# Optimization experiments

Measured on AMD Instinct MI355X. Metric: run time of the kernel, lower is better.

Reference implementation:

```python
import jax, jax.numpy as jnp
import numpy as np

B, L, IN, OUT = 32, 2048, 192, 2
H, N2, NL = 512, 32, 4  # hidden_dim, d_state//2 complex modes, num_layers


def setup_inputs() -> dict:
    key = jax.random.key(0)
    ks = jax.random.split(key, 8)
    neural_input = jax.random.normal(ks[0], (B, L, IN), jnp.float32)
    W_in = jax.random.normal(ks[1], (IN, H), jnp.float32) / np.sqrt(IN)
    b_in = jnp.zeros((H,), jnp.float32)
    # S4D kernel params (stacked over layers)
    log_dt = jax.random.uniform(ks[2], (NL, H), jnp.float32, np.log(1e-3), np.log(1e-1))
    Cri = jax.random.normal(ks[3], (NL, H, N2, 2), jnp.float32)  # complex C as (re, im)
    log_A_real = jnp.full((NL, H, N2), np.log(0.5), jnp.float32)
    A_imag = jnp.broadcast_to(np.pi * jnp.arange(N2, dtype=np.float32), (NL, H, N2)).astype(jnp.float32)
    D = jax.random.normal(ks[4], (NL, H), jnp.float32)
    # position-wise output conv1x1 producing 2H channels for GLU
    conv_w = jax.random.normal(ks[5], (NL, 2 * H, H), jnp.float32) / np.sqrt(H)
    conv_b = jnp.zeros((NL, 2 * H), jnp.float32)
    W_out = jax.random.normal(ks[6], (H, OUT), jnp.float32) / np.sqrt(H)
    b_out = jnp.zeros((OUT,), jnp.float32)
    return dict(neural_input=neural_input, W_in=W_in, b_in=b_in, log_dt=log_dt,
                Cri=Cri, log_A_real=log_A_real, A_imag=A_imag, D=D,
                conv_w=conv_w, conv_b=conv_b, W_out=W_out, b_out=b_out)


def _s4d_layer(u, log_dt, Cri, log_A_real, A_imag, D, conv_w, conv_b):
    # u: (B, H, L)
    Lx = u.shape[-1]
    dt = jnp.exp(log_dt)[:, None]                       # (H, 1)
    C = Cri[..., 0] + 1j * Cri[..., 1]                  # (H, N2) complex
    A = -jnp.exp(log_A_real) + 1j * A_imag              # (H, N2)
    dtA = A * dt                                        # (H, N2)
    Ct = C * (jnp.exp(dtA) - 1.0) / A                   # (H, N2)
    # Vandermonde kernel: K[h, l] = 2 Re sum_n Ct[h,n] exp(dtA[h,n] * l)
    vand = jnp.exp(dtA[..., None] * jnp.arange(Lx))     # (H, N2, L) complex
    K = 2.0 * jnp.einsum('hn,hnl->hl', Ct, vand).real   # (H, L)
    # circular conv via FFT at length 2L (== linear conv, causal)
    k_f = jnp.fft.rfft(K, n=2 * Lx)
    u_f = jnp.fft.rfft(u, n=2 * Lx)
    y = jnp.fft.irfft(u_f * k_f, n=2 * Lx)[..., :Lx]    # (B, H, L)
    y = y + u * D[:, None]
    y = jax.nn.gelu(y, approximate=False)               # torch nn.GELU (erf)
    # conv1x1 to 2H channels + GLU over channel dim
    z = jnp.einsum('oh,bhl->bol', conv_w, y) + conv_b[None, :, None]
    a, b = jnp.split(z, 2, axis=1)
    return a * jax.nn.sigmoid(b)


def reference(neural_input, W_in, b_in, log_dt, Cri, log_A_real, A_imag, D,
              conv_w, conv_b, W_out, b_out):
    x = neural_input @ W_in + b_in          # (B, L, H)
    u = jnp.transpose(x, (0, 2, 1))         # (B, H, L) channels-first for SSM
    for i in range(NL):
        u = _s4d_layer(u, log_dt[i], Cri[i], log_A_real[i], A_imag[i],
                       D[i], conv_w[i], conv_b[i])
    y = jnp.transpose(u, (0, 2, 1))         # (B, L, H)
    return y @ W_out + b_out                # (B, L, OUT)
```

## Files before the change

### kernel.cpp

```cpp
#include <hip/hip_runtime.h>
#include <hip/hip_bf16.h>
#include <math.h>

#define BB 32
#define LL 2048
#define INP 192
#define OUTC 2
#define HH 512
#define NN2 32
#define NNL 4
#define TABB 32768

using short8 = __attribute__((ext_vector_type(8))) short;
using f32x4  = __attribute__((ext_vector_type(4))) float;
using f32x2  = __attribute__((ext_vector_type(2))) float;

__device__ __forceinline__ float sigmoidf_(float x) {
  return 1.0f / (1.0f + expf(-x));
}
__device__ __forceinline__ unsigned short bf16bits(float x) {
  __hip_bfloat16 b = __float2bfloat16(x);
  return __builtin_bit_cast(unsigned short, b);
}
__device__ __forceinline__ float bfval(unsigned short b) {
  unsigned int u = (unsigned int)b << 16;
  return __builtin_bit_cast(float, u);
}
__device__ __forceinline__ float gelu_fast(float x) {
  float s = x * 0.70710678118654752f;
  float ax = fabsf(s);
  float tt = 1.0f / fmaf(0.3275911f, ax, 1.0f);
  float p = fmaf(1.061405429f, tt, -1.453152027f);
  p = fmaf(p, tt, 1.421413741f);
  p = fmaf(p, tt, -0.284496736f);
  p = fmaf(p, tt, 0.254829592f);
  float e = __expf(-s * s);
  float er = 1.0f - p * tt * e;
  er = copysignf(er, s);
  return 0.5f * x * (1.0f + er);
}
__device__ __forceinline__ void gload16(const void* gsrc, void* ldst) {
  __builtin_amdgcn_global_load_lds(
      (const __attribute__((address_space(1))) void*)gsrc,
      (__attribute__((address_space(3))) void*)ldst, 16, 0, 0);
}

__global__ __launch_bounds__(256) void k_params(const float* __restrict__ log_dt,
                                                const float* __restrict__ Cri,
                                                const float* __restrict__ lAr,
                                                const float* __restrict__ Aim,
                                                float* __restrict__ P) {
  int idx = blockIdx.x * 256 + threadIdx.x;
  if (idx >= NNL * HH * NN2) return;
  float dt  = expf(log_dt[idx / NN2]);
  float Are = -expf(lAr[idx]);
  float Aimv = Aim[idx];
  float dre = Are * dt, dim = Aimv * dt;
  float er = expf(dre);
  float wrv = er * cosf(dim);
  float wiv = er * sinf(dim);
  float Er = wrv - 1.0f, Ei = wiv;
  float den = Are * Are + Aimv * Aimv;
  float Fr = (Er * Are + Ei * Aimv) / den;
  float Fi = (Ei * Are - Er * Aimv) / den;
  float Cre = Cri[idx * 2 + 0], Cim = Cri[idx * 2 + 1];
  P[idx * 4 + 0] = wrv;
  P[idx * 4 + 1] = wiv;
  P[idx * 4 + 2] = 2.0f * (Cre * Fr - Cim * Fi);
  P[idx * 4 + 3] = 2.0f * (Cre * Fi + Cim * Fr);
}

__global__ __launch_bounds__(64) void k_tables(const float* __restrict__ P,
                                               char* __restrict__ Tab) {
  __shared__ float kk[32];
  int tid = threadIdx.x;
  int lh = blockIdx.x;
  char* tb = Tab + (size_t)lh * TABB;
  if (tid < 32) {
    int n = tid;
    const float4 pq = reinterpret_cast<const float4*>(P)[(size_t)lh * NN2 + n];
    float wr = pq.x, wi = pq.y, c2r = pq.z, c2i = pq.w;
    int mt = n >> 4;
    float pr = 1.0f, pi = 0.0f;
    for (int d = 0; d < 32; ++d) {
      {
        int t_ = 31 - d;
        int lane = ((t_ >> 3) << 4) + (n & 15);
        int j = t_ & 7;
        unsigned short hr = bf16bits(pr);
        unsigned short lr = bf16bits(pr - bfval(hr));
        unsigned short hi_ = bf16bits(pi);
        unsigned short li_ = bf16bits(pi - bfval(hi_));
        *(unsigned short*)(tb + (mt * 2 + 0) * 1024 + lane * 16 + j * 2) = hr;
        *(unsigned short*)(tb + (mt * 2 + 1) * 1024 + lane * 16 + j * 2) = hi_;
        *(unsigned short*)(tb + 4096 + (mt * 2 + 0) * 1024 + lane * 16 + j * 2) = lr;
        *(unsigned short*)(tb + 4096 + (mt * 2 + 1) * 1024 + lane * 16 + j * 2) = li_;
      }
      {
        int mtT = d >> 4;
        int lane = (((n & 15) >> 2) << 4) + (d & 15);
        int jre = n & 3, jim = (n & 3) + 4;
        unsigned short hr = bf16bits(pr);
        unsigned short lr = bf16bits(pr - bfval(hr));
        float nim = -pi;
        unsigned short hi_ = bf16bits(nim);
        unsigned short li_ = bf16bits(nim - bfval(hi_));
        char* bh = tb + 8192 + (mtT * 2 + mt) * 1024 + lane * 16;
        char* bl = tb + 12288 + (mtT * 2 + mt) * 1024 + lane * 16;
        *(unsigned short*)(bh + jre * 2) = hr;
        *(unsigned short*)(bh + jim * 2) = hi_;
        *(unsigned short*)(bl + jre * 2) = lr;
        *(unsigned short*)(bl + jim * 2) = li_;
      }
      float kp = c2r * pr - c2i * pi;
      #pragma unroll
      for (int k = 1; k < 32; k <<= 1) kp += __shfl_xor(kp, k, 32);
      if (n == 0) kk[d] = kp;
      float nr = pr * wr - pi * wi;
      pi = pr * wi + pi * wr;
      pr = nr;
    }
    float w32r = pr, w32i = pi;
    float c2wr = c2r * wr - c2i * wi;
    float c2wi = c2r * wi + c2i * wr;
    int s = ((n >> 4) << 2) + (n & 3);
    int gg = (n & 15) >> 2;
    float pmr = 1.0f, pmi = 0.0f;
    for (int m = 0; m < 16; ++m) {
      float* q = (float*)(tb + 20480 + (size_t)((s * 64) + (gg * 16 + m)) * 24);
      q[0] = w32r; q[1] = w32i; q[2] = pmr; q[3] = pmi; q[4] = c2wr; q[5] = c2wi;
      float t2 = pmr * w32r - pmi * w32i;
      pmi = pmr * w32i + pmi * w32r;
      pmr = t2;
    }
  }
  __syncthreads();
  for (int idx = tid; idx < 1024; idx += 64) {
    int mt = idx >> 9, rem = idx & 511;
    int lane = rem >> 3, j = rem & 7;
    int tt = (mt << 4) + (lane & 15);
    int jf = ((lane >> 4) << 3) + j;
    float val = (jf <= tt) ? kk[tt - jf] : 0.0f;
    unsigned short hb = bf16bits(val);
    unsigned short lb = bf16bits(val - bfval(hb));
    *(unsigned short*)(tb + 16384 + mt * 1024 + lane * 16 + j * 2) = hb;
    *(unsigned short*)(tb + 18432 + mt * 1024 + lane * 16 + j * 2) = lb;
  }
}

__global__ __launch_bounds__(256) void k_tobf16(const float* __restrict__ src,
                                                __hip_bfloat16* __restrict__ dst,
                                                int n) {
  int i = (blockIdx.x * 256 + threadIdx.x) * 4;
  if (i >= n) return;
  float4 v = *reinterpret_cast<const float4*>(&src[i]);
  dst[i + 0] = __float2bfloat16(v.x);
  dst[i + 1] = __float2bfloat16(v.y);
  dst[i + 2] = __float2bfloat16(v.z);
  dst[i + 3] = __float2bfloat16(v.w);
}

__global__ __launch_bounds__(256) void k_splitx(const float* __restrict__ src,
                                                __hip_bfloat16* __restrict__ hi,
                                                __hip_bfloat16* __restrict__ lo,
                                                int n) {
  int i = (blockIdx.x * 256 + threadIdx.x) * 4;
  if (i >= n) return;
  float4 v = *reinterpret_cast<const float4*>(&src[i]);
  float vv[4] = {v.x, v.y, v.z, v.w};
  unsigned short hb[4], lb[4];
  #pragma unroll
  for (int j = 0; j < 4; ++j) {
    hb[j] = bf16bits(vv[j]);
    lb[j] = bf16bits(vv[j] - bfval(hb[j]));
  }
  *reinterpret_cast<uint2*>(hi + i) = make_uint2(
      (unsigned)hb[0] | ((unsigned)hb[1] << 16), (unsigned)hb[2] | ((unsigned)hb[3] << 16));
  *reinterpret_cast<uint2*>(lo + i) = make_uint2(
      (unsigned)lb[0] | ((unsigned)lb[1] << 16), (unsigned)lb[2] | ((unsigned)lb[3] << 16));
}

__global__ __launch_bounds__(256) void k_prepwt(const float* __restrict__ W,
                                                __hip_bfloat16* __restrict__ hi,
                                                __hip_bfloat16* __restrict__ lo) {
  int idx = blockIdx.x * 256 + threadIdx.x;
  if (idx >= HH * INP) return;
  int h = idx / INP, k = idx - h * INP;
  float v = W[(size_t)k * HH + h];
  unsigned short hb = bf16bits(v);
  hi[idx] = __builtin_bit_cast(__hip_bfloat16, hb);
  lo[idx] = __float2bfloat16(v - bfval(hb));
}

__global__ __launch_bounds__(256) void k_ingemm(const __hip_bfloat16* __restrict__ Xhi,
                                                const __hip_bfloat16* __restrict__ Xlo,
                                                const __hip_bfloat16* __restrict__ Wthi,
                                                const __hip_bfloat16* __restrict__ Wtlo,
                                                const float* __restrict__ bias,
                                                float* __restrict__ U) {
  int lt = blockIdx.x * 128;
  int ht = blockIdx.y * 128;
  int b  = blockIdx.z;
  int t = threadIdx.x;
  int wid = t >> 6, lane = t & 63;
  int wrow = wid >> 1, wcol = wid & 1;
  int l15 = lane & 15, g = lane >> 4;

  const short* Xh = (const short*)Xhi + (size_t)b * LL * INP;
  const short* Xl = (const short*)Xlo + (size_t)b * LL * INP;
  const short* Bh = (const short*)Wthi;
  const short* Bl = (const short*)Wtlo;

  f32x4 acc[4][4];
  #pragma unroll
  for (int m = 0; m < 4; ++m)
    #pragma unroll
    for (int n = 0; n < 4; ++n) acc[m][n] = f32x4{0.f, 0.f, 0.f, 0.f};

  int lbase = lt + wrow * 64 + l15;
  int hbase = ht + wcol * 64 + l15;

  #pragma unroll
  for (int ks = 0; ks < 6; ++ks) {
    int k0 = ks * 32 + 8 * g;
    short8 ah[4], al[4], bh[4], bl[4];
    #pragma unroll
    for (int m = 0; m < 4; ++m) {
      size_t off = (size_t)(lbase + m * 16) * INP + k0;
      ah[m] = *reinterpret_cast<const short8*>(Xh + off);
      al[m] = *reinterpret_cast<const short8*>(Xl + off);
    }
    #pragma unroll
    for (int n = 0; n < 4; ++n) {
      size_t off = (size_t)(hbase + n * 16) * INP + k0;
      bh[n] = *reinterpret_cast<const short8*>(Bh + off);
      bl[n] = *reinterpret_cast<const short8*>(Bl + off);
    }
    #pragma unroll
    for (int m = 0; m < 4; ++m)
      #pragma unroll
      for (int n = 0; n < 4; ++n) {
        acc[m][n] = __builtin_amdgcn_mfma_f32_16x16x32_bf16(ah[m], bh[n], acc[m][n], 0, 0, 0);
        acc[m][n] = __builtin_amdgcn_mfma_f32_16x16x32_bf16(ah[m], bl[n], acc[m][n], 0, 0, 0);
        acc[m][n] = __builtin_amdgcn_mfma_f32_16x16x32_bf16(al[m], bh[n], acc[m][n], 0, 0, 0);
      }
  }

  #pragma unroll
  for (int n = 0; n < 4; ++n) {
    int h = hbase + n * 16;
    float bv = bias[h];
    #pragma unroll
    for (int m = 0; m < 4; ++m) {
      int l0 = lt + wrow * 64 + m * 16 + g * 4;
      float4 o;
      o.x = acc[m][n][0] + bv;
      o.y = acc[m][n][1] + bv;
      o.z = acc[m][n][2] + bv;
      o.w = acc[m][n][3] + bv;
      *reinterpret_cast<float4*>(&U[((size_t)b * HH + h) * LL + l0]) = o;
    }
  }
}

__global__ __launch_bounds__(512) void k_scan(const float* __restrict__ U,
                                              short* __restrict__ Ybt,
                                              const char* __restrict__ Tab,
                                              const float* __restrict__ Dp) {
  __shared__ short ylds[8 * 2048];
  int t = threadIdx.x;
  int lane = t & 63;
  int wid = t >> 6;
  int row = __builtin_amdgcn_readfirstlane(blockIdx.x * 8 + wid);
  int h = row & (HH - 1);
  const char* tb = Tab + (size_t)h * TABB;
  const float* urow = U + (size_t)row * LL;
  int g = lane >> 4, m = lane & 15;

  short8 uh[4], ul[4];
  #pragma unroll
  for (int c0 = 0; c0 < 4; ++c0) {
    const float* p = urow + 512 * c0 + 32 * m + 8 * g;
    float4 va = *reinterpret_cast<const float4*>(p);
    float4 vb = *reinterpret_cast<const float4*>(p + 4);
    float v[8] = {va.x, va.y, va.z, va.w, vb.x, vb.y, vb.z, vb.w};
    short8 hi, lo;
    #pragma unroll
    for (int j = 0; j < 8; ++j) {
      unsigned short hb = bf16bits(v[j]);
      hi[j] = (short)hb;
      lo[j] = (short)bf16bits(v[j] - bfval(hb));
    }
    uh[c0] = hi;
    ul[c0] = lo;
  }

  f32x4 Z[2][2][4];
  #pragma unroll
  for (int mt = 0; mt < 2; ++mt)
    #pragma unroll
    for (int reim = 0; reim < 2; ++reim) {
      short8 whi = *reinterpret_cast<const short8*>(tb + (mt * 2 + reim) * 1024 + lane * 16);
      short8 wlo = *reinterpret_cast<const short8*>(tb + 4096 + (mt * 2 + reim) * 1024 + lane * 16);
      #pragma unroll
      for (int c0 = 0; c0 < 4; ++c0) {
        f32x4 z = {0.f, 0.f, 0.f, 0.f};
        z = __builtin_amdgcn_mfma_f32_16x16x32_bf16(whi, uh[c0], z, 0, 0, 0);
        z = __builtin_amdgcn_mfma_f32_16x16x32_bf16(whi, ul[c0], z, 0, 0, 0);
        z = __builtin_amdgcn_mfma_f32_16x16x32_bf16(wlo, uh[c0], z, 0, 0, 0);
        Z[mt][reim][c0] = z;
      }
    }

  float aR[8][4], aI[8][4];
  #pragma unroll
  for (int s = 0; s < 8; ++s) {
    int mt = s >> 2, i = s & 3;
    const char* plb = tb + 20480 + (size_t)(s * 64 + lane) * 24;
    f32x2 w32 = *reinterpret_cast<const f32x2*>(plb);
    f32x2 w32m = *reinterpret_cast<const f32x2*>(plb + 8);
    f32x2 c2w = *reinterpret_cast<const f32x2*>(plb + 16);
    float r1r = w32[0], r1i = w32[1];
    float r2r = r1r * r1r - r1i * r1i, r2i = 2.f * r1r * r1i;
    float r4r = r2r * r2r - r2i * r2i, r4i = 2.f * r2r * r2i;
    float r8r = r4r * r4r - r4i * r4i, r8i = 2.f * r4r * r4i;
    float w16r = r8r * r8r - r8i * r8i, w16i = 2.f * r8r * r8i;

    float Er[4], Ei[4], Tr[4], Ti[4];
    #pragma unroll
    for (int c0 = 0; c0 < 4; ++c0) {
      float Pr = Z[mt][0][c0][i], Pi = Z[mt][1][c0][i];
      {
        float qr = __shfl_up(Pr, 1u, 16), qi = __shfl_up(Pi, 1u, 16);
        if (m < 1) { qr = 0.f; qi = 0.f; }
        Pr = fmaf(r1r, qr, fmaf(-r1i, qi, Pr));
        Pi = fmaf(r1r, qi, fmaf(r1i, qr, Pi));
      }
      {
        float qr = __shfl_up(Pr, 2u, 16), qi = __shfl_up(Pi, 2u, 16);
        if (m < 2) { qr = 0.f; qi = 0.f; }
        Pr = fmaf(r2r, qr, fmaf(-r2i, qi, Pr));
        Pi = fmaf(r2r, qi, fmaf(r2i, qr, Pi));
      }
      {
        float qr = __shfl_up(Pr, 4u, 16), qi = __shfl_up(Pi, 4u, 16);
        if (m < 4) { qr = 0.f; qi = 0.f; }
        Pr = fmaf(r4r, qr, fmaf(-r4i, qi, Pr));
        Pi = fmaf(r4r, qi, fmaf(r4i, qr, Pi));
      }
      {
        float qr = __shfl_up(Pr, 8u, 16), qi = __shfl_up(Pi, 8u, 16);
        if (m < 8) { qr = 0.f; qi = 0.f; }
        Pr = fmaf(r8r, qr, fmaf(-r8i, qi, Pr));
        Pi = fmaf(r8r, qi, fmaf(r8i, qr, Pi));
      }
      float eqr = __shfl_up(Pr, 1u, 16), eqi = __shfl_up(Pi, 1u, 16);
      if (m == 0) { eqr = 0.f; eqi = 0.f; }
      Er[c0] = eqr; Ei[c0] = eqi;
      Tr[c0] = __shfl(Pr, 15, 16);
      Ti[c0] = __shfl(Pi, 15, 16);
    }
    float C1r = Tr[0], C1i = Ti[0];
    float C2r = fmaf(w16r, C1r, fmaf(-w16i, C1i, Tr[1]));
    float C2i = fmaf(w16r, C1i, fmaf(w16i, C1r, Ti[1]));
    float C3r = fmaf(w16r, C2r, fmaf(-w16i, C2i, Tr[2]));
    float C3i = fmaf(w16r, C2i, fmaf(w16i, C2r, Ti[2]));
    float Cr[4] = {0.f, C1r, C2r, C3r};
    float Ci[4] = {0.f, C1i, C2i, C3i};
    #pragma unroll
    for (int c0 = 0; c0 < 4; ++c0) {
      float Erc = fmaf(w32m[0], Cr[c0], fmaf(-w32m[1], Ci[c0], Er[c0]));
      float Eic = fmaf(w32m[0], Ci[c0], fmaf(w32m[1], Cr[c0], Ei[c0]));
      aR[s][c0] = c2w[0] * Erc - c2w[1] * Eic;
      aI[s][c0] = c2w[0] * Eic + c2w[1] * Erc;
    }
  }

  short8 afh[2][4], afl[2][4];
  #pragma unroll
  for (int kt = 0; kt < 2; ++kt)
    #pragma unroll
    for (int c0 = 0; c0 < 4; ++c0) {
      float av[8] = {aR[kt * 4 + 0][c0], aR[kt * 4 + 1][c0], aR[kt * 4 + 2][c0], aR[kt * 4 + 3][c0],
                     aI[kt * 4 + 0][c0], aI[kt * 4 + 1][c0], aI[kt * 4 + 2][c0], aI[kt * 4 + 3][c0]};
      short8 hi, lo;
      #pragma unroll
      for (int j = 0; j < 8; ++j) {
        unsigned short hb = bf16bits(av[j]);
        hi[j] = (short)hb;
        lo[j] = (short)bf16bits(av[j] - bfval(hb));
      }
      afh[kt][c0] = hi;
      afl[kt][c0] = lo;
    }

  f32x4 y[2][4];
  #pragma unroll
  for (int mtT = 0; mtT < 2; ++mtT) {
    short8 fh = *reinterpret_cast<const short8*>(tb + 16384 + mtT * 1024 + lane * 16);
    short8 fl = *reinterpret_cast<const short8*>(tb + 18432 + mtT * 1024 + lane * 16);
    short8 wch0 = *reinterpret_cast<const short8*>(tb + 8192 + (mtT * 2 + 0) * 1024 + lane * 16);
    short8 wcl0 = *reinterpret_cast<const short8*>(tb + 12288 + (mtT * 2 + 0) * 1024 + lane * 16);
    short8 wch1 = *reinterpret_cast<const short8*>(tb + 8192 + (mtT * 2 + 1) * 1024 + lane * 16);
    short8 wcl1 = *reinterpret_cast<const short8*>(tb + 12288 + (mtT * 2 + 1) * 1024 + lane * 16);
    #pragma unroll
    for (int c0 = 0; c0 < 4; ++c0) {
      f32x4 acc = {0.f, 0.f, 0.f, 0.f};
      acc = __builtin_amdgcn_mfma_f32_16x16x32_bf16(fh, uh[c0], acc, 0, 0, 0);
      acc = __builtin_amdgcn_mfma_f32_16x16x32_bf16(fh, ul[c0], acc, 0, 0, 0);
      acc = __builtin_amdgcn_mfma_f32_16x16x32_bf16(fl, uh[c0], acc, 0, 0, 0);
      acc = __builtin_amdgcn_mfma_f32_16x16x32_bf16(wch0, afh[0][c0], acc, 0, 0, 0);
      acc = __builtin_amdgcn_mfma_f32_16x16x32_bf16(wch0, afl[0][c0], acc, 0, 0, 0);
      acc = __builtin_amdgcn_mfma_f32_16x16x32_bf16(wcl0, afh[0][c0], acc, 0, 0, 0);
      acc = __builtin_amdgcn_mfma_f32_16x16x32_bf16(wch1, afh[1][c0], acc, 0, 0, 0);
      acc = __builtin_amdgcn_mfma_f32_16x16x32_bf16(wch1, afl[1][c0], acc, 0, 0, 0);
      acc = __builtin_amdgcn_mfma_f32_16x16x32_bf16(wcl1, afh[1][c0], acc, 0, 0, 0);
      y[mtT][c0] = acc;
    }
  }

  float Dv = Dp[h];
  #pragma unroll
  for (int mtT = 0; mtT < 2; ++mtT)
    #pragma unroll
    for (int c0 = 0; c0 < 4; ++c0) {
      int eb = 512 * c0 + 32 * m + 16 * mtT + 4 * g;
      float4 uu = *reinterpret_cast<const float4*>(urow + eb);
      f32x4 vv = y[mtT][c0];
      unsigned short bv[4];
      bv[0] = bf16bits(gelu_fast(fmaf(Dv, uu.x, vv[0])));
      bv[1] = bf16bits(gelu_fast(fmaf(Dv, uu.y, vv[1])));
      bv[2] = bf16bits(gelu_fast(fmaf(Dv, uu.z, vv[2])));
      bv[3] = bf16bits(gelu_fast(fmaf(Dv, uu.w, vv[3])));
      int ymask = ((eb >> 5) & 7) << 4;
      #pragma unroll
      for (int k = 0; k < 4; ++k) {
        *(short*)((char*)ylds + (((eb + k) * 16 + wid * 2) ^ ymask)) = (short)bv[k];
      }
    }
  __syncthreads();
  #pragma unroll
  for (int i = 0; i < 4; ++i) {
    int l = t + 512 * i;
    int ymask = ((l >> 5) & 7) << 4;
    uint4 v = *reinterpret_cast<const uint4*>((const char*)ylds + ((l * 16) ^ ymask));
    *reinterpret_cast<uint4*>(Ybt + ((size_t)blockIdx.x * 2048 + l) * 8) = v;
  }
}

__global__ __launch_bounds__(256) void k_conv(const short* __restrict__ Ybt,
                                              const __hip_bfloat16* __restrict__ CWb,
                                              const float* __restrict__ CB,
                                              float* __restrict__ U) {
  __shared__ short Alds[128 * 64];
  int lt = blockIdx.x * 128;
  int ot = blockIdx.y * 64;
  int b  = blockIdx.z;
  int t = threadIdx.x;
  int wid = t >> 6, lane = t & 63;
  int wr = wid >> 1, wc = wid & 1;
  int l15 = lane & 15, l4 = lane >> 4;
  f32x4 zero = {0.f, 0.f, 0.f, 0.f};
  f32x4 accA[2][4], accG[2][4];
  #pragma unroll
  for (int m = 0; m < 2; ++m)
    #pragma unroll
    for (int n = 0; n < 4; ++n) { accA[m][n] = zero; accG[m][n] = zero; }

  const short* Yb = Ybt + (size_t)b * 64 * 2048 * 8;
  const char* Wb = (const char*)CWb;

  for (int kt = 0; kt < HH; kt += 64) {
    #pragma unroll
    for (int it = 0; it < 4; ++it) {
      int d = 16 * (t + 256 * it);
      int rowl = d >> 7, cb = d & 127;
      int orow = (rowl < 64) ? (ot + rowl) : (448 + ot + rowl);
      gload16(Wb + (size_t)orow * 1024 + kt * 2 + (cb ^ ((rowl & 7) << 4)),
              (char*)Alds + d);
    }
    short8 bfrag[2][4];
    #pragma unroll
    for (int ks = 0; ks < 2; ++ks)
      #pragma unroll
      for (int n = 0; n < 4; ++n) {
        int l = lt + wc * 64 + n * 16 + l15;
        int octg = (kt >> 3) + ks * 4 + l4;
        bfrag[ks][n] = *reinterpret_cast<const short8*>(
            Yb + ((size_t)octg * 2048 + l) * 8);
      }
    __syncthreads();
    #pragma unroll
    for (int ks = 0; ks < 2; ++ks) {
      short8 af[4];
      #pragma unroll
      for (int m = 0; m < 4; ++m) {
        int mrow = ((m < 2) ? (wr * 32 + m * 16) : (64 + wr * 32 + (m - 2) * 16)) + l15;
        int colb = (ks * 64 + 16 * l4) ^ ((mrow & 7) << 4);
        af[m] = *reinterpret_cast<const short8*>((const char*)Alds + mrow * 128 + colb);
      }
      #pragma unroll
      for (int m = 0; m < 2; ++m)
        #pragma unroll
        for (int n = 0; n < 4; ++n) {
          accA[m][n] = __builtin_amdgcn_mfma_f32_16x16x32_bf16(af[m], bfrag[ks][n], accA[m][n], 0, 0, 0);
          accG[m][n] = __builtin_amdgcn_mfma_f32_16x16x32_bf16(af[m + 2], bfrag[ks][n], accG[m][n], 0, 0, 0);
        }
    }
    __syncthreads();
  }
  #pragma unroll
  for (int m = 0; m < 2; ++m) {
    #pragma unroll
    for (int r = 0; r < 4; ++r) {
      int rowl = wr * 32 + m * 16 + l4 * 4 + r;
      float ba = CB[ot + rowl];
      float bg = CB[512 + ot + rowl];
      float* urow_ = U + ((size_t)b * HH + ot + rowl) * LL + lt + wc * 64;
      #pragma unroll
      for (int n = 0; n < 4; ++n) {
        float a = accA[m][n][r] + ba;
        float g = accG[m][n][r] + bg;
        urow_[n * 16 + l15] = a * sigmoidf_(g);
      }
    }
  }
}

__global__ __launch_bounds__(256) void k_outgemm(const float* __restrict__ U,
                                                 const float* __restrict__ Wo,
                                                 const float* __restrict__ bo,
                                                 float* __restrict__ out) {
  int bl = blockIdx.x * 256 + threadIdx.x;
  int b = bl >> 11, l = bl & (LL - 1);
  float a0 = 0.0f, a1 = 0.0f;
  const float* up = U + (size_t)b * HH * LL + l;
  #pragma unroll 4
  for (int h = 0; h < HH; ++h) {
    float v = up[(size_t)h * LL];
    a0 = fmaf(v, Wo[h * 2 + 0], a0);
    a1 = fmaf(v, Wo[h * 2 + 1], a1);
  }
  out[(size_t)bl * 2 + 0] = a0 + bo[0];
  out[(size_t)bl * 2 + 1] = a1 + bo[1];
}

extern "C" void kernel_launch(void* const* d_in, const int* in_sizes, int n_in,
                              void* d_out, int out_size, void* d_ws, size_t ws_size,
                              hipStream_t stream) {
  const float* X      = (const float*)d_in[0];
  const float* Win    = (const float*)d_in[1];
  const float* bin    = (const float*)d_in[2];
  const float* log_dt = (const float*)d_in[3];
  const float* Cri    = (const float*)d_in[4];
  const float* lAr    = (const float*)d_in[5];
  const float* Aim    = (const float*)d_in[6];
  const float* Dp     = (const float*)d_in[7];
  const float* CW     = (const float*)d_in[8];
  const float* CB     = (const float*)d_in[9];
  const float* Wo     = (const float*)d_in[10];
  const float* bo     = (const float*)d_in[11];
  float* out = (float*)d_out;

  const size_t Pfloats   = (size_t)NNL * HH * NN2 * 4;
  const size_t CWfloats  = (size_t)NNL * 2 * HH * HH / 2;
  const size_t Tabfloats = (size_t)NNL * HH * (TABB / 4);
  const size_t Wtfloats  = (size_t)HH * INP;
  const size_t Xnf       = (size_t)BB * LL * INP;
  const size_t HL        = (size_t)HH * LL;

  float* P = (float*)d_ws;
  __hip_bfloat16* CWb = (__hip_bfloat16*)(P + Pfloats);
  char* Tab = (char*)(P + Pfloats + CWfloats);
  __hip_bfloat16* Wthi = (__hip_bfloat16*)(P + Pfloats + CWfloats + Tabfloats);
  __hip_bfloat16* Wtlo = Wthi + Wtfloats;
  __hip_bfloat16* Xhi  = (__hip_bfloat16*)(P + Pfloats + CWfloats + Tabfloats + Wtfloats);
  __hip_bfloat16* Xlo  = Xhi + Xnf;
  size_t head = Pfloats + CWfloats + Tabfloats + Wtfloats + Xnf;

  size_t ws_floats = ws_size / sizeof(float);
  size_t avail = (ws_floats > head) ? (ws_floats - head) : 0;
  int G = (int)(avail / (HL + HL / 2));
  if (G >= 32) G = 32;
  else if (G >= 16) G = 16;
  else if (G >= 8) G = 8;
  else if (G >= 4) G = 4;
  else if (G >= 2) G = 2;
  else G = 1;

  float* U = P + head;
  short* Ybt = (short*)(U + (size_t)G * HL);

  k_params<<<(NNL * HH * NN2 + 255) / 256, 256, 0, stream>>>(log_dt, Cri, lAr, Aim, P);
  k_tables<<<NNL * HH, 64, 0, stream>>>(P, Tab);
  k_tobf16<<<(NNL * 2 * HH * HH) / 1024, 256, 0, stream>>>(CW, CWb, NNL * 2 * HH * HH);
  k_prepwt<<<(HH * INP + 255) / 256, 256, 0, stream>>>(Win, Wthi, Wtlo);
  k_splitx<<<(int)(Xnf / 1024), 256, 0, stream>>>(X, Xhi, Xlo, (int)Xnf);

  for (int b0 = 0; b0 < BB; b0 += G) {
    int g = (BB - b0 < G) ? (BB - b0) : G;
    k_ingemm<<<dim3(LL / 128, HH / 128, g), 256, 0, stream>>>(
        Xhi + (size_t)b0 * LL * INP, Xlo + (size_t)b0 * LL * INP, Wthi, Wtlo, bin, U);
    for (int layer = 0; layer < NNL; ++layer) {
      k_scan<<<g * (HH / 8), 512, 0, stream>>>(
          U, Ybt,
          Tab + (size_t)layer * HH * TABB,
          Dp + (size_t)layer * HH);
      k_conv<<<dim3(LL / 128, HH / 64, g), 256, 0, stream>>>(
          Ybt, CWb + (size_t)layer * 2 * HH * HH, CB + (size_t)layer * 2 * HH, U);
    }
    k_outgemm<<<g * LL / 256, 256, 0, stream>>>(
        U, Wo, bo, out + (size_t)b0 * LL * OUTC);
  }
}
```

Before: 1.236 ms.

## Shrink scan blocks, stage u hi-bits in LDS, interleave Z and prefix stages

The scan kernel now runs 4 waves per block instead of 8, with a launch-bounds occupancy hint of 6. The bf16 high part of u is kept in shared memory instead of registers, and the Z MFMA stage is fused with the prefix-scan stage per k-tile, so only half of the Z and a values are live at once. The intent is to cut register pressure and raise occupancy. The Ybt layout changes to groups of 4 channels, so the conv kernel now assembles its B fragments from two 8-byte loads, which costs extra memory transactions in that kernel.

New measurement: 2.293 ms. 1.85x slower.

```diff
diff --git a/kernel.cpp b/kernel.cpp
--- a/kernel.cpp
+++ b/kernel.cpp
@@ -14,6 +14,8 @@
 using short8 = __attribute__((ext_vector_type(8))) short;
 using f32x4  = __attribute__((ext_vector_type(4))) float;
 using f32x2  = __attribute__((ext_vector_type(2))) float;
+
+struct u2x2 { uint2 a, b; };
 
 __device__ __forceinline__ float sigmoidf_(float x) {
   return 1.0f / (1.0f + expf(-x));
@@ -263,21 +265,22 @@
   }
 }
 
-__global__ __launch_bounds__(512) void k_scan(const float* __restrict__ U,
-                                              short* __restrict__ Ybt,
-                                              const char* __restrict__ Tab,
-                                              const float* __restrict__ Dp) {
-  __shared__ short ylds[8 * 2048];
+__global__ __launch_bounds__(256, 6) void k_scan(const float* __restrict__ U,
+                                                 short* __restrict__ Ybt,
+                                                 const char* __restrict__ Tab,
+                                                 const float* __restrict__ Dp) {
+  __shared__ __align__(16) char smem[16384];
   int t = threadIdx.x;
   int lane = t & 63;
   int wid = t >> 6;
-  int row = __builtin_amdgcn_readfirstlane(blockIdx.x * 8 + wid);
+  int row = __builtin_amdgcn_readfirstlane(blockIdx.x * 4 + wid);
   int h = row & (HH - 1);
   const char* tb = Tab + (size_t)h * TABB;
   const float* urow = U + (size_t)row * LL;
   int g = lane >> 4, m = lane & 15;
-
-  short8 uh[4], ul[4];
+  char* ubase = smem + wid * 4096;
+
+  short8 ul[4];
   #pragma unroll
   for (int c0 = 0; c0 < 4; ++c0) {
     const float* p = urow + 512 * c0 + 32 * m + 8 * g;
@@ -291,98 +294,95 @@
       hi[j] = (short)hb;
       lo[j] = (short)bf16bits(v[j] - bfval(hb));
     }
-    uh[c0] = hi;
+    *reinterpret_cast<short8*>(ubase + c0 * 1024 + lane * 16) = hi;
     ul[c0] = lo;
   }
 
-  f32x4 Z[2][2][4];
-  #pragma unroll
-  for (int mt = 0; mt < 2; ++mt)
+  short8 afh[2][4], afl[2][4];
+  #pragma unroll
+  for (int kt = 0; kt < 2; ++kt) {
+    f32x4 Z[2][4];
     #pragma unroll
     for (int reim = 0; reim < 2; ++reim) {
-      short8 whi = *reinterpret_cast<const short8*>(tb + (mt * 2 + reim) * 1024 + lane * 16);
-      short8 wlo = *reinterpret_cast<const short8*>(tb + 4096 + (mt * 2 + reim) * 1024 + lane * 16);
+      short8 whi = *reinterpret_cast<const short8*>(tb + (kt * 2 + reim) * 1024 + lane * 16);
+      short8 wlo = *reinterpret_cast<const short8*>(tb + 4096 + (kt * 2 + reim) * 1024 + lane * 16);
       #pragma unroll
       for (int c0 = 0; c0 < 4; ++c0) {
+        short8 uhv = *reinterpret_cast<const short8*>(ubase + c0 * 1024 + lane * 16);
         f32x4 z = {0.f, 0.f, 0.f, 0.f};
-        z = __builtin_amdgcn_mfma_f32_16x16x32_bf16(whi, uh[c0], z, 0, 0, 0);
+        z = __builtin_amdgcn_mfma_f32_16x16x32_bf16(whi, uhv, z, 0, 0, 0);
         z = __builtin_amdgcn_mfma_f32_16x16x32_bf16(whi, ul[c0], z, 0, 0, 0);
-        z = __builtin_amdgcn_mfma_f32_16x16x32_bf16(wlo, uh[c0], z, 0, 0, 0);
-        Z[mt][reim][c0] = z;
-      }
-    }
-
-  float aR[8][4], aI[8][4];
-  #pragma unroll
-  for (int s = 0; s < 8; ++s) {
-    int mt = s >> 2, i = s & 3;
-    const char* plb = tb + 20480 + (size_t)(s * 64 + lane) * 24;
-    f32x2 w32 = *reinterpret_cast<const f32x2*>(plb);
-    f32x2 w32m = *reinterpret_cast<const f32x2*>(plb + 8);
-    f32x2 c2w = *reinterpret_cast<const f32x2*>(plb + 16);
-    float r1r = w32[0], r1i = w32[1];
-    float r2r = r1r * r1r - r1i * r1i, r2i = 2.f * r1r * r1i;
-    float r4r = r2r * r2r - r2i * r2i, r4i = 2.f * r2r * r2i;
-    float r8r = r4r * r4r - r4i * r4i, r8i = 2.f * r4r * r4i;
-    float w16r = r8r * r8r - r8i * r8i, w16i = 2.f * r8r * r8i;
-
-    float Er[4], Ei[4], Tr[4], Ti[4];
+        z = __builtin_amdgcn_mfma_f32_16x16x32_bf16(wlo, uhv, z, 0, 0, 0);
+        Z[reim][c0] = z;
+      }
+    }
+    float aR[4][4], aI[4][4];
+    #pragma unroll
+    for (int i = 0; i < 4; ++i) {
+      int s = kt * 4 + i;
+      const char* plb = tb + 20480 + (size_t)(s * 64 + lane) * 24;
+      f32x2 w32 = *reinterpret_cast<const f32x2*>(plb);
+      f32x2 w32m = *reinterpret_cast<const f32x2*>(plb + 8);
+      f32x2 c2w = *reinterpret_cast<const f32x2*>(plb + 16);
+      float r1r = w32[0], r1i = w32[1];
+      float r2r = r1r * r1r - r1i * r1i, r2i = 2.f * r1r * r1i;
+      float r4r = r2r * r2r - r2i * r2i, r4i = 2.f * r2r * r2i;
+      float r8r = r4r * r4r - r4i * r4i, r8i = 2.f * r4r * r4i;
+      float w16r = r8r * r8r - r8i * r8i, w16i = 2.f * r8r * r8i;
+
+      float Er[4], Ei[4], Tr[4], Ti[4];
+      #pragma unroll
+      for (int c0 = 0; c0 < 4; ++c0) {
+        float Pr = Z[0][c0][i], Pi = Z[1][c0][i];
+        {
+          float qr = __shfl_up(Pr, 1u, 16), qi = __shfl_up(Pi, 1u, 16);
+          if (m < 1) { qr = 0.f; qi = 0.f; }
+          Pr = fmaf(r1r, qr, fmaf(-r1i, qi, Pr));
+          Pi = fmaf(r1r, qi, fmaf(r1i, qr, Pi));
+        }
+        {
+          float qr = __shfl_up(Pr, 2u, 16), qi = __shfl_up(Pi, 2u, 16);
+          if (m < 2) { qr = 0.f; qi = 0.f; }
+          Pr = fmaf(r2r, qr, fmaf(-r2i, qi, Pr));
+          Pi = fmaf(r2r, qi, fmaf(r2i, qr, Pi));
+        }
+        {
+          float qr = __shfl_up(Pr, 4u, 16), qi = __shfl_up(Pi, 4u, 16);
+          if (m < 4) { qr = 0.f; qi = 0.f; }
+          Pr = fmaf(r4r, qr, fmaf(-r4i, qi, Pr));
+          Pi = fmaf(r4r, qi, fmaf(r4i, qr, Pi));
+        }
+        {
+          float qr = __shfl_up(Pr, 8u, 16), qi = __shfl_up(Pi, 8u, 16);
+          if (m < 8) { qr = 0.f; qi = 0.f; }
+          Pr = fmaf(r8r, qr, fmaf(-r8i, qi, Pr));
+          Pi = fmaf(r8r, qi, fmaf(r8i, qr, Pi));
+        }
+        float eqr = __shfl_up(Pr, 1u, 16), eqi = __shfl_up(Pi, 1u, 16);
+        if (m == 0) { eqr = 0.f; eqi = 0.f; }
+        Er[c0] = eqr; Ei[c0] = eqi;
+        Tr[c0] = __shfl(Pr, 15, 16);
+        Ti[c0] = __shfl(Pi, 15, 16);
+      }
+      float C1r = Tr[0], C1i = Ti[0];
+      float C2r = fmaf(w16r, C1r, fmaf(-w16i, C1i, Tr[1]));
+      float C2i = fmaf(w16r, C1i, fmaf(w16i, C1r, Ti[1]));
+      float C3r = fmaf(w16r, C2r, fmaf(-w16i, C2i, Tr[2]));
+      float C3i = fmaf(w16r, C2i, fmaf(w16i, C2r, Ti[2]));
+      float Cr[4] = {0.f, C1r, C2r, C3r};
+      float Ci[4] = {0.f, C1i, C2i, C3i};
+      #pragma unroll
+      for (int c0 = 0; c0 < 4; ++c0) {
+        float Erc = fmaf(w32m[0], Cr[c0], fmaf(-w32m[1], Ci[c0], Er[c0]));
+        float Eic = fmaf(w32m[0], Ci[c0], fmaf(w32m[1], Cr[c0], Ei[c0]));
+        aR[i][c0] = c2w[0] * Erc - c2w[1] * Eic;
+        aI[i][c0] = c2w[0] * Eic + c2w[1] * Erc;
+      }
+    }
     #pragma unroll
     for (int c0 = 0; c0 < 4; ++c0) {
-      float Pr = Z[mt][0][c0][i], Pi = Z[mt][1][c0][i];
-      {
-        float qr = __shfl_up(Pr, 1u, 16), qi = __shfl_up(Pi, 1u, 16);
-        if (m < 1) { qr = 0.f; qi = 0.f; }
-        Pr = fmaf(r1r, qr, fmaf(-r1i, qi, Pr));
-        Pi = fmaf(r1r, qi, fmaf(r1i, qr, Pi));
-      }
-      {
-        float qr = __shfl_up(Pr, 2u, 16), qi = __shfl_up(Pi, 2u, 16);
-        if (m < 2) { qr = 0.f; qi = 0.f; }
-        Pr = fmaf(r2r, qr, fmaf(-r2i, qi, Pr));
-        Pi = fmaf(r2r, qi, fmaf(r2i, qr, Pi));
-      }
-      {
-        float qr = __shfl_up(Pr, 4u, 16), qi = __shfl_up(Pi, 4u, 16);
-        if (m < 4) { qr = 0.f; qi = 0.f; }
-        Pr = fmaf(r4r, qr, fmaf(-r4i, qi, Pr));
-        Pi = fmaf(r4r, qi, fmaf(r4i, qr, Pi));
-      }
-      {
-        float qr = __shfl_up(Pr, 8u, 16), qi = __shfl_up(Pi, 8u, 16);
-        if (m < 8) { qr = 0.f; qi = 0.f; }
-        Pr = fmaf(r8r, qr, fmaf(-r8i, qi, Pr));
-        Pi = fmaf(r8r, qi, fmaf(r8i, qr, Pi));
-      }
-      float eqr = __shfl_up(Pr, 1u, 16), eqi = __shfl_up(Pi, 1u, 16);
-      if (m == 0) { eqr = 0.f; eqi = 0.f; }
-      Er[c0] = eqr; Ei[c0] = eqi;
-      Tr[c0] = __shfl(Pr, 15, 16);
-      Ti[c0] = __shfl(Pi, 15, 16);
-    }
-    float C1r = Tr[0], C1i = Ti[0];
-    float C2r = fmaf(w16r, C1r, fmaf(-w16i, C1i, Tr[1]));
-    float C2i = fmaf(w16r, C1i, fmaf(w16i, C1r, Ti[1]));
-    float C3r = fmaf(w16r, C2r, fmaf(-w16i, C2i, Tr[2]));
-    float C3i = fmaf(w16r, C2i, fmaf(w16i, C2r, Ti[2]));
-    float Cr[4] = {0.f, C1r, C2r, C3r};
-    float Ci[4] = {0.f, C1i, C2i, C3i};
-    #pragma unroll
-    for (int c0 = 0; c0 < 4; ++c0) {
-      float Erc = fmaf(w32m[0], Cr[c0], fmaf(-w32m[1], Ci[c0], Er[c0]));
-      float Eic = fmaf(w32m[0], Ci[c0], fmaf(w32m[1], Cr[c0], Ei[c0]));
-      aR[s][c0] = c2w[0] * Erc - c2w[1] * Eic;
-      aI[s][c0] = c2w[0] * Eic + c2w[1] * Erc;
-    }
-  }
-
-  short8 afh[2][4], afl[2][4];
-  #pragma unroll
-  for (int kt = 0; kt < 2; ++kt)
-    #pragma unroll
-    for (int c0 = 0; c0 < 4; ++c0) {
-      float av[8] = {aR[kt * 4 + 0][c0], aR[kt * 4 + 1][c0], aR[kt * 4 + 2][c0], aR[kt * 4 + 3][c0],
-                     aI[kt * 4 + 0][c0], aI[kt * 4 + 1][c0], aI[kt * 4 + 2][c0], aI[kt * 4 + 3][c0]};
+      float av[8] = {aR[0][c0], aR[1][c0], aR[2][c0], aR[3][c0],
+                     aI[0][c0], aI[1][c0], aI[2][c0], aI[3][c0]};
       short8 hi, lo;
       #pragma unroll
       for (int j = 0; j < 8; ++j) {
@@ -393,6 +393,7 @@
       afh[kt][c0] = hi;
       afl[kt][c0] = lo;
     }
+  }
 
   f32x4 y[2][4];
   #pragma unroll
@@ -405,10 +406,11 @@
     short8 wcl1 = *reinterpret_cast<const short8*>(tb + 12288 + (mtT * 2 + 1) * 1024 + lane * 16);
     #pragma unroll
     for (int c0 = 0; c0 < 4; ++c0) {
+      short8 uhv = *reinterpret_cast<const short8*>(ubase + c0 * 1024 + lane * 16);
       f32x4 acc = {0.f, 0.f, 0.f, 0.f};
-      acc = __builtin_amdgcn_mfma_f32_16x16x32_bf16(fh, uh[c0], acc, 0, 0, 0);
+      acc = __builtin_amdgcn_mfma_f32_16x16x32_bf16(fh, uhv, acc, 0, 0, 0);
       acc = __builtin_amdgcn_mfma_f32_16x16x32_bf16(fh, ul[c0], acc, 0, 0, 0);
-      acc = __builtin_amdgcn_mfma_f32_16x16x32_bf16(fl, uh[c0], acc, 0, 0, 0);
+      acc = __builtin_amdgcn_mfma_f32_16x16x32_bf16(fl, uhv, acc, 0, 0, 0);
       acc = __builtin_amdgcn_mfma_f32_16x16x32_bf16(wch0, afh[0][c0], acc, 0, 0, 0);
       acc = __builtin_amdgcn_mfma_f32_16x16x32_bf16(wch0, afl[0][c0], acc, 0, 0, 0);
       acc = __builtin_amdgcn_mfma_f32_16x16x32_bf16(wcl0, afh[0][c0], acc, 0, 0, 0);
@@ -418,6 +420,8 @@
       y[mtT][c0] = acc;
     }
   }
+
+  __syncthreads();
 
   float Dv = Dp[h];
   #pragma unroll
@@ -432,19 +436,18 @@
       bv[1] = bf16bits(gelu_fast(fmaf(Dv, uu.y, vv[1])));
       bv[2] = bf16bits(gelu_fast(fmaf(Dv, uu.z, vv[2])));
       bv[3] = bf16bits(gelu_fast(fmaf(Dv, uu.w, vv[3])));
-      int ymask = ((eb >> 5) & 7) << 4;
       #pragma unroll
       for (int k = 0; k < 4; ++k) {
-        *(short*)((char*)ylds + (((eb + k) * 16 + wid * 2) ^ ymask)) = (short)bv[k];
+        int l = eb + k;
+        *(short*)(smem + ((l * 8 + wid * 2) ^ (((l >> 4) & 7) << 3))) = (short)bv[k];
       }
     }
   __syncthreads();
   #pragma unroll
-  for (int i = 0; i < 4; ++i) {
-    int l = t + 512 * i;
-    int ymask = ((l >> 5) & 7) << 4;
-    uint4 v = *reinterpret_cast<const uint4*>((const char*)ylds + ((l * 16) ^ ymask));
-    *reinterpret_cast<uint4*>(Ybt + ((size_t)blockIdx.x * 2048 + l) * 8) = v;
+  for (int i = 0; i < 8; ++i) {
+    int l = t + 256 * i;
+    uint2 v = *reinterpret_cast<const uint2*>(smem + ((l * 8) ^ (((l >> 4) & 7) << 3)));
+    *reinterpret_cast<uint2*>(Ybt + ((size_t)blockIdx.x * 2048 + l) * 4) = v;
   }
 }
 
@@ -467,7 +470,7 @@
     #pragma unroll
     for (int n = 0; n < 4; ++n) { accA[m][n] = zero; accG[m][n] = zero; }
 
-  const short* Yb = Ybt + (size_t)b * 64 * 2048 * 8;
+  const short* Yb = Ybt + (size_t)b * 128 * 2048 * 4;
   const char* Wb = (const char*)CWb;
 
   for (int kt = 0; kt < HH; kt += 64) {
@@ -486,8 +489,10 @@
       for (int n = 0; n < 4; ++n) {
         int l = lt + wc * 64 + n * 16 + l15;
         int octg = (kt >> 3) + ks * 4 + l4;
-        bfrag[ks][n] = *reinterpret_cast<const short8*>(
-            Yb + ((size_t)octg * 2048 + l) * 8);
+        const short* p0 = Yb + ((size_t)(2 * octg) * 2048 + l) * 4;
+        uint2 A = *reinterpret_cast<const uint2*>(p0);
+        uint2 B2 = *reinterpret_cast<const uint2*>(p0 + 8192);
+        bfrag[ks][n] = __builtin_bit_cast(short8, u2x2{A, B2});
       }
     __syncthreads();
     #pragma unroll
@@ -602,7 +607,7 @@
     k_ingemm<<<dim3(LL / 128, HH / 128, g), 256, 0, stream>>>(
         Xhi + (size_t)b0 * LL * INP, Xlo + (size_t)b0 * LL * INP, Wthi, Wtlo, bin, U);
     for (int layer = 0; layer < NNL; ++layer) {
-      k_scan<<<g * (HH / 8), 512, 0, stream>>>(
+      k_scan<<<g * (HH / 4), 256, 0, stream>>>(
           U, Ybt,
           Tab + (size_t)layer * HH * TABB,
           Dp + (size_t)layer * HH);
```
